# Optimization experiments

Hardware: AMD Instinct MI355X
Metric: run time of the kernel (lower is better)

Reference implementation:

```python
import jax, jax.numpy as jnp
import numpy as np

B, H, S, D = 4, 16, 2048, 128


def setup_inputs() -> dict:
    key = jax.random.key(0)
    kq, kk, kv, km = jax.random.split(key, 4)
    queries = jax.random.normal(kq, (B, H, S, D), dtype=jnp.float32)
    keys = jax.random.normal(kk, (B, H, S, D), dtype=jnp.float32)
    values = jax.random.normal(kv, (B, H, S, D), dtype=jnp.float32)
    # 0/1 float mask (1 = masked position), broadcast over heads
    mask = jax.random.randint(km, (B, 1, S, S), 0, 2).astype(jnp.float32)
    return {"queries": queries, "keys": keys, "values": values, "mask": mask}


def reference(queries, keys, values, mask):
    dk = jnp.asarray(keys.shape[-1], dtype=queries.dtype)
    # NOTE: original code divides by dk, not sqrt(dk) — kept faithful.
    scores = jnp.einsum("bhqd,bhkd->bhqk", queries, keys) / dk
    scores = scores + mask * jnp.asarray(-1e9, dtype=scores.dtype)
    attn = jax.nn.softmax(scores, axis=-1)
    out = jnp.einsum("bhqk,bhkd->bhqd", attn, values)
    return out, attn
```

## Files before the change

### kernel.cpp

```cpp
#include <hip/hip_runtime.h>

#define Bb 4
#define Hh 16
#define Ss 2048
#define Dd 128
#define KT 32
#define NIT (Ss / KT)

typedef __bf16 bf16x8 __attribute__((ext_vector_type(8)));
typedef __bf16 bf16x4 __attribute__((ext_vector_type(4)));
typedef float f32x4 __attribute__((ext_vector_type(4)));

__global__ void k_cvt(const float4* __restrict__ Q, const float4* __restrict__ K,
                      bf16x4* __restrict__ Qb, bf16x4* __restrict__ Kb) {
    size_t i = (size_t)blockIdx.x * 256 + threadIdx.x;
    float4 q = Q[i], k = K[i];
    Qb[i] = (bf16x4){(__bf16)q.x, (__bf16)q.y, (__bf16)q.z, (__bf16)q.w};
    Kb[i] = (bf16x4){(__bf16)k.x, (__bf16)k.y, (__bf16)k.z, (__bf16)k.w};
}

__global__ void k_vt(const float* __restrict__ V, __bf16* __restrict__ VT) {
    __shared__ __bf16 lds[64][65];
    int k0 = blockIdx.x * 64, d0 = blockIdx.y * 64, bh = blockIdx.z;
    int t = threadIdx.x;
    for (int i = 0; i < 16; ++i) {
        int idx = i * 256 + t;
        int kl = idx >> 6, dl = idx & 63;
        lds[kl][dl] = (__bf16)V[((size_t)(bh * Ss + k0 + kl)) * Dd + d0 + dl];
    }
    __syncthreads();
    for (int i = 0; i < 16; ++i) {
        int idx = i * 256 + t;
        int dl = idx >> 6, kl = idx & 63;
        VT[((size_t)(bh * Dd + d0 + dl)) * Ss + k0 + kl] = lds[kl][dl];
    }
}

__global__ void k_mask(const float* __restrict__ M, unsigned* __restrict__ maskT) {
    __shared__ unsigned char lds[64][68];
    int k0 = blockIdx.x * 64, q0 = blockIdx.y * 64, b = blockIdx.z;
    int t = threadIdx.x;
    for (int i = 0; i < 16; ++i) {
        int idx = i * 256 + t;
        int ql = idx >> 6, kl = idx & 63;
        lds[ql][kl] = (M[((size_t)(b * Ss + q0 + ql)) * Ss + k0 + kl] != 0.0f) ? 1 : 0;
    }
    __syncthreads();
    if (t < 128) {
        int kl = t >> 1, wsel = t & 1;
        unsigned wv = 0;
        for (int j = 0; j < 32; ++j)
            wv |= ((unsigned)lds[wsel * 32 + j][kl]) << j;
        maskT[((size_t)(b * Ss + k0 + kl)) * (Ss / 32) + (q0 >> 5) + wsel] = wv;
    }
}

__device__ __forceinline__ void gl2lds16(const void* g, void* l) {
    __builtin_amdgcn_global_load_lds(
        (const __attribute__((address_space(1))) unsigned int*)g,
        (__attribute__((address_space(3))) unsigned int*)l, 16, 0, 0);
}

__global__ __launch_bounds__(256, 4) void attn_kernel(
    const __bf16* __restrict__ Qb, const __bf16* __restrict__ Kb,
    const __bf16* __restrict__ VTb, const unsigned* __restrict__ maskT,
    float* __restrict__ out, float* __restrict__ attn) {
    __shared__ __align__(16) __bf16 Ks[2][KT][Dd];
    __shared__ __align__(16) __bf16 VTs[2][Dd][KT];
    __shared__ __align__(16) __bf16 Ps[4][16][64];

    const int t = threadIdx.x;
    const int w = t >> 6, lane = t & 63, quad = lane >> 4, l16 = lane & 15;

    const int wg = (int)blockIdx.x + ((int)blockIdx.y << 5);
    const int nid = ((wg & 7) << 8) + (wg >> 3);
    const int q0 = (nid & 31) << 6;
    const int bh = nid >> 5;
    const int b = bh >> 4;

    const __bf16* Kbh = Kb + (size_t)bh * (Ss * Dd);
    const char* Vbh = (const char*)(VTb + (size_t)bh * ((size_t)Dd * Ss));

    const int ksub = t >> 4;
    const int kcb = ((t & 15) << 4) ^ ((ksub & 7) << 4);
    const int vsub = t >> 2;
    const int vcb = ((t & 3) << 4) ^ ((vsub & 3) << 4);
    char* ldsKbase = (char*)&Ks[0][0][0] + (w << 10);
    char* ldsVbase = (char*)&VTs[0][0][0] + (w << 10);

#define STAGE_K(buf, k0_)                                                      \
    {                                                                          \
        const char* gb = (const char*)(Kbh + (size_t)(k0_) * Dd) + kcb;        \
        _Pragma("unroll") for (int i_ = 0; i_ < 2; ++i_)                       \
            gl2lds16(gb + ((i_ << 4) + ksub) * 256,                            \
                     ldsKbase + ((buf) << 13) + (i_ << 12));                   \
    }
#define STAGE_V(buf, k0_)                                                      \
    {                                                                          \
        const char* gb = Vbh + (size_t)(k0_) * 2 + vcb;                        \
        _Pragma("unroll") for (int i_ = 0; i_ < 2; ++i_)                       \
            gl2lds16(gb + (size_t)((i_ << 6) + vsub) * (Ss * 2),               \
                     ldsVbase + ((buf) << 13) + (i_ << 12));                   \
    }

    bf16x8 aq[4];
    {
        STAGE_K(0, 0);
        const __bf16* qp =
            Qb + ((size_t)(bh * Ss + q0 + (w << 4) + l16)) * Dd + (quad << 3);
#pragma unroll
        for (int kd = 0; kd < 4; ++kd) aq[kd] = *(const bf16x8*)(qp + (kd << 5));
    }
    __syncthreads();

    const char* ldsK0 = (const char*)&Ks[0][0][0];
    const char* ldsV0 = (const char*)&VTs[0][0][0];
    const int kswz = (l16 & 7) << 4;
    const int vswz = (l16 & 3) << 4;

    const int qw = (q0 >> 5) + (w >> 1);
    const int bitbase = ((w & 1) << 4) + (quad << 2);
    const size_t mrowbase = (size_t)b * Ss * (Ss / 32);

    float rsum[4] = {0.f, 0.f, 0.f, 0.f};
    for (int it = 0; it < NIT; ++it) {
        const int cur = it & 1;
        if (it < NIT - 1) {
            STAGE_K(cur ^ 1, (it + 1) * KT);
        } else {
            STAGE_K(cur ^ 1, 0);
            STAGE_V(cur ^ 1, 0);
        }
        const int k0 = it * KT;
#pragma unroll
        for (int nt = 0; nt < 2; ++nt) {
            f32x4 acc = {0.f, 0.f, 0.f, 0.f};
#pragma unroll
            for (int kd = 0; kd < 4; ++kd) {
                bf16x8 bk = *(const bf16x8*)(ldsK0 + (cur << 13) +
                                             ((nt * 16 + l16) << 8) +
                                             (((kd << 6) + (quad << 4)) ^ kswz));
                acc = __builtin_amdgcn_mfma_f32_16x16x32_bf16(aq[kd], bk, acc, 0, 0, 0);
            }
            const int col = k0 + nt * 16 + l16;
            const unsigned mw = maskT[mrowbase + (size_t)col * (Ss / 32) + qw];
#pragma unroll
            for (int r = 0; r < 4; ++r)
                rsum[r] += ((mw >> (bitbase + r)) & 1u) ? 0.f
                                                        : __expf(acc[r] * 0.0078125f);
        }
        __syncthreads();
    }

    float li[4];
#pragma unroll
    for (int r = 0; r < 4; ++r) {
        float v = rsum[r];
        v += __shfl_xor(v, 1, 16);
        v += __shfl_xor(v, 2, 16);
        v += __shfl_xor(v, 4, 16);
        v += __shfl_xor(v, 8, 16);
        li[r] = 1.0f / v;
    }

    f32x4 oacc[8];
#pragma unroll
    for (int dg = 0; dg < 8; ++dg) oacc[dg] = (f32x4){0.f, 0.f, 0.f, 0.f};

    char* myPs = (char*)&Ps[0][0][0] + (w << 11);

    for (int it = 0; it < NIT; ++it) {
        const int cur = it & 1;
        if (it < NIT - 1) {
            STAGE_K(cur ^ 1, (it + 1) * KT);
            STAGE_V(cur ^ 1, (it + 1) * KT);
        }
        const int k0 = it * KT;
#pragma unroll
        for (int nt = 0; nt < 2; ++nt) {
            f32x4 acc = {0.f, 0.f, 0.f, 0.f};
#pragma unroll
            for (int kd = 0; kd < 4; ++kd) {
                bf16x8 bk = *(const bf16x8*)(ldsK0 + (cur << 13) +
                                             ((nt * 16 + l16) << 8) +
                                             (((kd << 6) + (quad << 4)) ^ kswz));
                acc = __builtin_amdgcn_mfma_f32_16x16x32_bf16(aq[kd], bk, acc, 0, 0, 0);
            }
            const int col = k0 + nt * 16 + l16;
            const unsigned mw = maskT[mrowbase + (size_t)col * (Ss / 32) + qw];
#pragma unroll
            for (int r = 0; r < 4; ++r) {
                const int prow = (quad << 2) + r;
                float p = ((mw >> (bitbase + r)) & 1u)
                              ? 0.0f
                              : __expf(acc[r] * 0.0078125f) * li[r];
                attn[((size_t)(bh * Ss + q0 + (w << 4) + prow)) * Ss + col] = p;
                *(__bf16*)(myPs + (prow << 7) +
                           ((nt * 32 + (l16 << 1)) ^ ((prow & 7) << 4))) = (__bf16)p;
            }
        }
        {
            bf16x8 ap = *(const bf16x8*)(myPs + (l16 << 7) + ((quad << 4) ^ kswz));
#pragma unroll
            for (int dg = 0; dg < 8; ++dg) {
                bf16x8 bv = *(const bf16x8*)(ldsV0 + (cur << 13) +
                                             ((dg * 16 + l16) << 6) +
                                             ((quad << 4) ^ vswz));
                oacc[dg] = __builtin_amdgcn_mfma_f32_16x16x32_bf16(ap, bv, oacc[dg], 0, 0, 0);
            }
        }
        __syncthreads();
    }

#pragma unroll
    for (int dg = 0; dg < 8; ++dg)
#pragma unroll
        for (int r = 0; r < 4; ++r)
            out[((size_t)(bh * Ss + q0 + (w << 4) + (quad << 2) + r)) * Dd + dg * 16 +
                l16] = oacc[dg][r];
}

extern "C" void kernel_launch(void* const* d_in, const int* in_sizes, int n_in,
                              void* d_out, int out_size, void* d_ws, size_t ws_size,
                              hipStream_t stream) {
    const float* Q = (const float*)d_in[0];
    const float* K = (const float*)d_in[1];
    const float* V = (const float*)d_in[2];
    const float* M = (const float*)d_in[3];

    float* out = (float*)d_out;
    float* attn = out + (size_t)Bb * Hh * Ss * Dd;

    char* ws = (char*)d_ws;
    __bf16* Qb = (__bf16*)ws;
    __bf16* Kb = (__bf16*)(ws + 33554432);
    __bf16* VTb = (__bf16*)(ws + 67108864);
    unsigned* maskT = (unsigned*)(ws + 100663296);

    k_cvt<<<16384, 256, 0, stream>>>((const float4*)Q, (const float4*)K,
                                     (bf16x4*)Qb, (bf16x4*)Kb);
    k_vt<<<dim3(32, 2, 64), 256, 0, stream>>>(V, VTb);
    k_mask<<<dim3(32, 32, 4), 256, 0, stream>>>(M, maskT);
    attn_kernel<<<dim3(32, 64), 256, 0, stream>>>(Qb, Kb, VTb, maskT, out, attn);
}
```

Measured before the change: 1.784 ms.

## Prefetch mask words a tile ahead, raise MFMA priority, relax loop barrier

Mask words for the next key tile are loaded one iteration early into registers, so the global mask load latency overlaps the current tile's work. MFMA sections are wrapped in s_setprio to favour matrix issue across waves. In the output loop, __syncthreads is replaced by a partial s_waitcnt vmcnt(8) plus a raw s_barrier, so the attention-probability stores can stay in flight across iterations. This relies on the exact count of outstanding vector memory ops. If the staging loads are miscounted, it could cause hazards.

New measurement: 1.680 ms. 5.9% less time.

```diff
diff --git a/kernel.cpp b/kernel.cpp
--- a/kernel.cpp
+++ b/kernel.cpp
@@ -121,20 +121,26 @@
     const int qw = (q0 >> 5) + (w >> 1);
     const int bitbase = ((w & 1) << 4) + (quad << 2);
     const size_t mrowbase = (size_t)b * Ss * (Ss / 32);
+    const unsigned* mbase = maskT + mrowbase + (size_t)l16 * (Ss / 32) + qw;
+#define MASK_AT(it_, nt_) mbase[((it_)*KT + (nt_)*16) * (Ss / 32)]
 
     float rsum[4] = {0.f, 0.f, 0.f, 0.f};
+    unsigned mc0 = MASK_AT(0, 0), mc1 = MASK_AT(0, 1);
     for (int it = 0; it < NIT; ++it) {
         const int cur = it & 1;
+        const int itn = (it + 1 < NIT) ? it + 1 : 0;
+        unsigned mn0 = MASK_AT(itn, 0);
+        unsigned mn1 = MASK_AT(itn, 1);
         if (it < NIT - 1) {
             STAGE_K(cur ^ 1, (it + 1) * KT);
         } else {
             STAGE_K(cur ^ 1, 0);
             STAGE_V(cur ^ 1, 0);
         }
-        const int k0 = it * KT;
 #pragma unroll
         for (int nt = 0; nt < 2; ++nt) {
             f32x4 acc = {0.f, 0.f, 0.f, 0.f};
+            __builtin_amdgcn_s_setprio(1);
 #pragma unroll
             for (int kd = 0; kd < 4; ++kd) {
                 bf16x8 bk = *(const bf16x8*)(ldsK0 + (cur << 13) +
@@ -142,14 +148,16 @@
                                              (((kd << 6) + (quad << 4)) ^ kswz));
                 acc = __builtin_amdgcn_mfma_f32_16x16x32_bf16(aq[kd], bk, acc, 0, 0, 0);
             }
-            const int col = k0 + nt * 16 + l16;
-            const unsigned mw = maskT[mrowbase + (size_t)col * (Ss / 32) + qw];
+            __builtin_amdgcn_s_setprio(0);
+            const unsigned mw = nt ? mc1 : mc0;
 #pragma unroll
             for (int r = 0; r < 4; ++r)
                 rsum[r] += ((mw >> (bitbase + r)) & 1u) ? 0.f
                                                         : __expf(acc[r] * 0.0078125f);
         }
         __syncthreads();
+        mc0 = mn0;
+        mc1 = mn1;
     }
 
     float li[4];
@@ -169,8 +177,13 @@
 
     char* myPs = (char*)&Ps[0][0][0] + (w << 11);
 
+    mc0 = MASK_AT(0, 0);
+    mc1 = MASK_AT(0, 1);
     for (int it = 0; it < NIT; ++it) {
         const int cur = it & 1;
+        const int itn = (it + 1 < NIT) ? it + 1 : 0;
+        unsigned mn0 = MASK_AT(itn, 0);
+        unsigned mn1 = MASK_AT(itn, 1);
         if (it < NIT - 1) {
             STAGE_K(cur ^ 1, (it + 1) * KT);
             STAGE_V(cur ^ 1, (it + 1) * KT);
@@ -179,6 +192,7 @@
 #pragma unroll
         for (int nt = 0; nt < 2; ++nt) {
             f32x4 acc = {0.f, 0.f, 0.f, 0.f};
+            __builtin_amdgcn_s_setprio(1);
 #pragma unroll
             for (int kd = 0; kd < 4; ++kd) {
                 bf16x8 bk = *(const bf16x8*)(ldsK0 + (cur << 13) +
@@ -186,8 +200,9 @@
                                              (((kd << 6) + (quad << 4)) ^ kswz));
                 acc = __builtin_amdgcn_mfma_f32_16x16x32_bf16(aq[kd], bk, acc, 0, 0, 0);
             }
+            __builtin_amdgcn_s_setprio(0);
             const int col = k0 + nt * 16 + l16;
-            const unsigned mw = maskT[mrowbase + (size_t)col * (Ss / 32) + qw];
+            const unsigned mw = nt ? mc1 : mc0;
 #pragma unroll
             for (int r = 0; r < 4; ++r) {
                 const int prow = (quad << 2) + r;
@@ -201,6 +216,7 @@
         }
         {
             bf16x8 ap = *(const bf16x8*)(myPs + (l16 << 7) + ((quad << 4) ^ kswz));
+            __builtin_amdgcn_s_setprio(1);
 #pragma unroll
             for (int dg = 0; dg < 8; ++dg) {
                 bf16x8 bv = *(const bf16x8*)(ldsV0 + (cur << 13) +
@@ -208,8 +224,13 @@
                                              ((quad << 4) ^ vswz));
                 oacc[dg] = __builtin_amdgcn_mfma_f32_16x16x32_bf16(ap, bv, oacc[dg], 0, 0, 0);
             }
-        }
-        __syncthreads();
+            __builtin_amdgcn_s_setprio(0);
+        }
+        asm volatile("s_waitcnt vmcnt(8)" ::: "memory");
+        __builtin_amdgcn_s_barrier();
+        __builtin_amdgcn_sched_barrier(0);
+        mc0 = mn0;
+        mc1 = mn1;
     }
 
 #pragma unroll
```
